# Performance work log

Hardware: AMD Instinct MI355X
Metric: run time of the kernel (lower is better)

## Reference

```python
import jax, jax.numpy as jnp
import numpy as np

B, S, D, H, DFF = 8, 1024, 1024, 16, 4096
DK = D // H
EPS = 1e-6
NEG = -1e9


def setup_inputs() -> dict:
    key = jax.random.key(0)
    ks = jax.random.split(key, 8)
    x = jax.random.normal(ks[0], (B, S, D), dtype=jnp.float32)
    mask = jnp.ones((B, 1, 1, S), dtype=jnp.int32)
    s = 0.02
    wq = jax.random.normal(ks[1], (D, D), jnp.float32) * s
    wk = jax.random.normal(ks[2], (D, D), jnp.float32) * s
    wv = jax.random.normal(ks[3], (D, D), jnp.float32) * s
    wo = jax.random.normal(ks[4], (D, D), jnp.float32) * s
    bq = jnp.zeros((D,), jnp.float32); bk = jnp.zeros((D,), jnp.float32)
    bv = jnp.zeros((D,), jnp.float32); bo = jnp.zeros((D,), jnp.float32)
    w1 = jax.random.normal(ks[5], (D, DFF), jnp.float32) * s
    b1 = jnp.zeros((DFF,), jnp.float32)
    w2 = jax.random.normal(ks[6], (DFF, D), jnp.float32) * s
    b2 = jnp.zeros((D,), jnp.float32)
    g1 = jnp.array(1.0, jnp.float32); be1 = jnp.array(0.0, jnp.float32)
    g2 = jnp.array(1.0, jnp.float32); be2 = jnp.array(0.0, jnp.float32)
    return dict(x=x, mask=mask, wq=wq, bq=bq, wk=wk, bk=bk, wv=wv, bv=bv,
                wo=wo, bo=bo, w1=w1, b1=b1, w2=w2, b2=b2,
                g1=g1, be1=be1, g2=g2, be2=be2)


def layer_norm(x, gamma, beta):
    # repo quirk: unbiased std (ddof=1), scalar gamma/beta, divide by (std+eps)
    mean = jnp.mean(x, axis=-1, keepdims=True)
    std = jnp.std(x, axis=-1, keepdims=True, ddof=1)
    return gamma * (x - mean) / (std + EPS) + beta


def mha(x, mask, wq, bq, wk, bk, wv, bv, wo, bo):
    q = (x @ wq + bq).reshape(B, S, H, DK).transpose(0, 2, 1, 3)  # bhsd
    k = (x @ wk + bk).reshape(B, S, H, DK).transpose(0, 2, 1, 3)
    v = (x @ wv + bv).reshape(B, S, H, DK).transpose(0, 2, 1, 3)
    scores = jnp.einsum('bhqd,bhkd->bhqk', q, k) / jnp.sqrt(jnp.float32(DK))
    scores = jnp.where(mask == 0, NEG, scores)
    attn = jax.nn.softmax(scores, axis=-1)
    out = jnp.einsum('bhqk,bhkd->bhqd', attn, v)
    out = out.transpose(0, 2, 1, 3).reshape(B, S, D)
    return out @ wo + bo


def reference(x, mask, wq, bq, wk, bk, wv, bv, wo, bo, w1, b1, w2, b2, g1, be1, g2, be2):
    # pre-LN residual: x + sublayer(norm(x)); dropout inert at eval
    x = x + mha(layer_norm(x, g1, be1), mask, wq, bq, wk, bk, wv, bv, wo, bo)
    h = layer_norm(x, g2, be2)
    x = x + (jax.nn.relu(h @ w1 + b1) @ w2 + b2)
    return x
```

## Files before the change

### kernel.cpp

```cpp
#include <hip/hip_runtime.h>
#include <math.h>

typedef __bf16 bf16;
typedef float f32x4 __attribute__((ext_vector_type(4)));
typedef float f32x16 __attribute__((ext_vector_type(16)));
typedef bf16 bf16x8 __attribute__((ext_vector_type(8)));
typedef bf16 bf16x4 __attribute__((ext_vector_type(4)));
typedef unsigned int u32;
typedef unsigned int u32x2 __attribute__((ext_vector_type(2)));

#define DEV __device__ __forceinline__

constexpr int Ss = 1024, Dd = 1024;
constexpr float EPSf = 1e-6f;
constexpr float SM_SCALE = 0.125f * 1.4426950408889634f;

DEV void gl_lds16(const void* g, void* l) {
  __builtin_amdgcn_global_load_lds(
      (const __attribute__((address_space(1))) void*)g,
      (__attribute__((address_space(3))) void*)l, 16, 0, 0);
}

DEV u32 cvtpk(float lo, float hi) {
  u32 r;
  asm("v_cvt_pk_bf16_f32 %0, %1, %2" : "=v"(r) : "v"(lo), "v"(hi));
  return r;
}

__global__ __launch_bounds__(256) void transpose6_k(
    const float* __restrict__ i0, const float* __restrict__ i1,
    const float* __restrict__ i2, const float* __restrict__ i3,
    const float* __restrict__ i4, const float* __restrict__ i5,
    bf16* __restrict__ o0, bf16* __restrict__ o1, bf16* __restrict__ o2,
    bf16* __restrict__ o3, bf16* __restrict__ o4, bf16* __restrict__ o5) {
  __shared__ float t[64 * 65];
  const int bi = blockIdx.x;
  const float* in;
  bf16* out;
  int R, C, local, sh;
  if (bi < 1024) {
    const int j = bi >> 8;
    local = bi & 255; R = 1024; C = 1024; sh = 4;
    in = (j == 0) ? i0 : (j == 1) ? i1 : (j == 2) ? i2 : i3;
    out = (j == 0) ? o0 : (j == 1) ? o1 : (j == 2) ? o2 : o3;
  } else if (bi < 2048) {
    local = bi - 1024; R = 1024; C = 4096; sh = 6; in = i4; out = o4;
  } else {
    local = bi - 2048; R = 4096; C = 1024; sh = 4; in = i5; out = o5;
  }
  const int nx = 1 << sh;
  const int bx = local & (nx - 1), by = local >> sh;
  const int tid = threadIdx.x;
  const int tx = tid & 63, ty = tid >> 6;
  const int r0 = by * 64, c0 = bx * 64;
#pragma unroll
  for (int i = 0; i < 16; i++) {
    int r = ty + i * 4;
    t[r * 65 + tx] = in[(size_t)(r0 + r) * C + c0 + tx];
  }
  __syncthreads();
#pragma unroll
  for (int i = 0; i < 16; i++) {
    int r = ty + i * 4;
    out[(size_t)(c0 + r) * R + r0 + tx] = (bf16)t[tx * 65 + r];
  }
}

__global__ __launch_bounds__(256) void ln_kernel(
    const float* __restrict__ in, bf16* __restrict__ out,
    const float* __restrict__ gp, const float* __restrict__ bp) {
  const int row = blockIdx.x;
  const int tid = threadIdx.x;
  float v[4];
  const float* p = in + (size_t)row * Dd + tid * 4;
#pragma unroll
  for (int i = 0; i < 4; i++) v[i] = p[i];
  float s = v[0] + v[1] + v[2] + v[3];
  float s2 = v[0] * v[0] + v[1] * v[1] + v[2] * v[2] + v[3] * v[3];
#pragma unroll
  for (int m = 1; m < 64; m <<= 1) {
    s += __shfl_xor(s, m, 64);
    s2 += __shfl_xor(s2, m, 64);
  }
  __shared__ float ls[4], ls2[4];
  if ((tid & 63) == 0) {
    ls[tid >> 6] = s;
    ls2[tid >> 6] = s2;
  }
  __syncthreads();
  s = ls[0] + ls[1] + ls[2] + ls[3];
  s2 = ls2[0] + ls2[1] + ls2[2] + ls2[3];
  float mean = s * (1.0f / Dd);
  float var = (s2 - (float)Dd * mean * mean) * (1.0f / (Dd - 1));
  var = fmaxf(var, 0.0f);
  float g = gp[0], be = bp[0];
  float rs = g / (sqrtf(var) + EPSf);
  bf16* q = out + (size_t)row * Dd + tid * 4;
#pragma unroll
  for (int i = 0; i < 4; i++) q[i] = (bf16)((v[i] - mean) * rs + be);
}

template <int EPI, int BK>
__global__ __launch_bounds__(256) void gemm_bt(
    const bf16* __restrict__ A, const bf16* __restrict__ Bt,
    const float* __restrict__ bias, const float* __restrict__ bias2,
    const float* __restrict__ bias3, const float* __restrict__ resid,
    bf16* __restrict__ vtb, void* __restrict__ Cout, int M, int N, int K,
    int sa, int sb) {
  __shared__ __attribute__((aligned(16))) char smem[2 * 128 * BK * 2];
  bf16* As = (bf16*)smem;
  bf16* Bs = (bf16*)(smem + 128 * BK * 2);
  constexpr int CPR = BK / 8;
  constexpr int RPJ = 256 / CPR;
  constexpr int NJ = BK / 16;
  const int tid = threadIdx.x;
  const int ln = tid & 63;
  const int wv = tid >> 6;
  const int wm = wv >> 1, wn = wv & 1;
  const int quad = ln >> 4, l16 = ln & 15;
  const int l7 = l16 & 7;
  const int nxg = gridDim.x;
  const int d = blockIdx.y * nxg + blockIdx.x;
  const int sseq = d >> 3;
  const int bxr = sseq % nxg;
  const int byr = (d & 7) + 8 * (sseq / nxg);
  const int m0 = byr * 128, n0 = bxr * 128;

  f32x4 acc[4][4];
#pragma unroll
  for (int i = 0; i < 4; i++)
#pragma unroll
    for (int j = 0; j < 4; j++) acc[i][j] = {0.f, 0.f, 0.f, 0.f};

  const int sr = tid / CPR;
  const int sc = (tid & (CPR - 1)) ^ (sr & 7);
  const size_t abase = (size_t)(m0 + sr) * sa + sc * 8;
  const size_t bbase = (size_t)(n0 + sr) * sb + sc * 8;

  for (int k0 = 0; k0 < K; k0 += BK) {
#pragma unroll
    for (int j = 0; j < NJ; j++) {
      gl_lds16(A + abase + (size_t)(j * RPJ) * sa + k0,
               (char*)As + j * 4096 + wv * 1024);
      gl_lds16(Bt + bbase + (size_t)(j * RPJ) * sb + k0,
               (char*)Bs + j * 4096 + wv * 1024);
    }
    __syncthreads();
#pragma unroll
    for (int kh = 0; kh < BK / 32; kh++) {
      bf16x8 af[4], bfr[4];
#pragma unroll
      for (int mi = 0; mi < 4; mi++)
        af[mi] = *(const bf16x8*)&As[(wm * 64 + mi * 16 + l16) * BK +
                                     ((kh * 4 + quad) ^ l7) * 8];
#pragma unroll
      for (int ni = 0; ni < 4; ni++)
        bfr[ni] = *(const bf16x8*)&Bs[(wn * 64 + ni * 16 + l16) * BK +
                                      ((kh * 4 + quad) ^ l7) * 8];
#pragma unroll
      for (int mi = 0; mi < 4; mi++)
#pragma unroll
        for (int ni = 0; ni < 4; ni++)
          acc[mi][ni] = __builtin_amdgcn_mfma_f32_16x16x32_bf16(
              af[mi], bfr[ni], acc[mi][ni], 0, 0, 0);
    }
    __syncthreads();
  }

  if constexpr (EPI == 4) {
    if (n0 < 2048) {
#pragma unroll
      for (int mi = 0; mi < 4; mi++) {
        const int m = m0 + wm * 64 + mi * 16 + quad * 4;
#pragma unroll
        for (int ni = 0; ni < 4; ni++) {
          const int n = n0 + wn * 64 + ni * 16 + l16;
          const float bvl = (n < 1024) ? bias[n] : bias2[n - 1024];
#pragma unroll
          for (int r = 0; r < 4; r++)
            ((bf16*)Cout)[(size_t)(m + r) * N + n] =
                (bf16)(acc[mi][ni][r] + bvl);
        }
      }
    } else {
      bf16* T = (bf16*)smem;
#pragma unroll
      for (int mi = 0; mi < 4; mi++) {
        const int ml = wm * 64 + mi * 16 + quad * 4;
        const int c = ml >> 3, hf = (ml >> 2) & 1;
#pragma unroll
        for (int ni = 0; ni < 4; ni++) {
          const int nl = wn * 64 + ni * 16 + l16;
          const float bvl = bias3[(n0 - 2048) + nl];
          bf16x4 tv;
#pragma unroll
          for (int r = 0; r < 4; r++) tv[r] = (bf16)(acc[mi][ni][r] + bvl);
          *(bf16x4*)&T[nl * 128 + ((c ^ (nl & 15)) << 3) + (hf << 2)] = tv;
        }
      }
      __syncthreads();
      const size_t vbase =
          ((size_t)(m0 >> 10) * 1024 + (n0 - 2048)) * Ss + (m0 & 1023);
#pragma unroll
      for (int p = 0; p < 8; p++) {
        const int row = p * 16 + (tid >> 4);
        const int k = tid & 15;
        bf16x8 vv = *(const bf16x8*)&T[row * 128 + ((k ^ (row & 15)) << 3)];
        *(bf16x8*)&vtb[vbase + (size_t)row * Ss + k * 8] = vv;
      }
    }
  } else {
#pragma unroll
    for (int mi = 0; mi < 4; mi++) {
      const int m = m0 + wm * 64 + mi * 16 + quad * 4;
#pragma unroll
      for (int ni = 0; ni < 4; ni++) {
        const int n = n0 + wn * 64 + ni * 16 + l16;
        float bvl = 0.0f;
        if constexpr (EPI != 3) bvl = bias[n];
#pragma unroll
        for (int r = 0; r < 4; r++) {
          float val = acc[mi][ni][r] + bvl;
          const size_t idx = (size_t)(m + r) * N + n;
          if constexpr (EPI == 1) {
            ((float*)Cout)[idx] = val + resid[idx];
          } else if constexpr (EPI == 2) {
            ((bf16*)Cout)[idx] = (bf16)fmaxf(val, 0.0f);
          } else {
            ((float*)Cout)[idx] = val + resid[idx];
          }
        }
      }
    }
  }
}

__global__ __launch_bounds__(512) void gemm256_relu(
    const bf16* __restrict__ A, const bf16* __restrict__ Bt,
    const float* __restrict__ bias, bf16* __restrict__ Cout, int M, int N,
    int K, int sa, int sb) {
  __shared__ __attribute__((aligned(16))) char smem[131072];
  const int tid = threadIdx.x;
  const int ln = tid & 63;
  const int wv = tid >> 6;
  const int wm = wv >> 2, wn = wv & 3;
  const int quad = ln >> 4, l16 = ln & 15;
  const int l7 = l16 & 7;
  const int nxg = gridDim.x;
  const int d = blockIdx.y * nxg + blockIdx.x;
  const int sseq = d >> 3;
  const int bxr = sseq % nxg;
  const int byr = (d & 7) + 8 * (sseq / nxg);
  const int m0 = byr * 256, n0 = bxr * 256;

  f32x4 acc[8][4];
#pragma unroll
  for (int i = 0; i < 8; i++)
#pragma unroll
    for (int j = 0; j < 4; j++) acc[i][j] = {0.f, 0.f, 0.f, 0.f};

  const int sr = tid >> 3;
  const int sc = (tid & 7) ^ (sr & 7);
  const size_t abase = (size_t)(m0 + sr) * sa + sc * 8;
  const size_t bbase = (size_t)(n0 + sr) * sb + sc * 8;
  const int w8 = tid >> 6;

  const int nt = K >> 6;
  int cur = 0;

  {
#pragma unroll
    for (int j = 0; j < 4; j++) {
      gl_lds16(A + abase + (size_t)(j * 64) * sa,
               smem + j * 8192 + w8 * 1024);
      gl_lds16(Bt + bbase + (size_t)(j * 64) * sb,
               smem + 32768 + j * 8192 + w8 * 1024);
    }
  }

  for (int t = 0; t < nt; ++t) {
    if (t + 1 < nt) {
      char* ldst = smem + (cur ^ 1) * 65536;
      const int koff = (t + 1) * 64;
#pragma unroll
      for (int j = 0; j < 4; j++) {
        gl_lds16(A + abase + (size_t)(j * 64) * sa + koff,
                 ldst + j * 8192 + w8 * 1024);
        gl_lds16(Bt + bbase + (size_t)(j * 64) * sb + koff,
                 ldst + 32768 + j * 8192 + w8 * 1024);
      }
      asm volatile("s_waitcnt vmcnt(8)" ::: "memory");
    } else {
      asm volatile("s_waitcnt vmcnt(0)" ::: "memory");
    }
    __builtin_amdgcn_s_barrier();

    const bf16* As = (const bf16*)(smem + cur * 65536);
    const bf16* Bs = (const bf16*)(smem + cur * 65536 + 32768);
    bf16x8 bfr[4][2];
#pragma unroll
    for (int ni = 0; ni < 4; ni++)
#pragma unroll
      for (int kh = 0; kh < 2; kh++)
        bfr[ni][kh] = *(const bf16x8*)&Bs[(wn * 64 + ni * 16 + l16) * 64 +
                                          (((kh * 4 + quad) ^ l7) * 8)];
#pragma unroll
    for (int p = 0; p < 4; p++) {
      bf16x8 af[2][2];
#pragma unroll
      for (int m2 = 0; m2 < 2; m2++)
#pragma unroll
        for (int kh = 0; kh < 2; kh++)
          af[m2][kh] =
              *(const bf16x8*)&As[(wm * 128 + (p * 2 + m2) * 16 + l16) * 64 +
                                  (((kh * 4 + quad) ^ l7) * 8)];
      __builtin_amdgcn_s_setprio(1);
#pragma unroll
      for (int m2 = 0; m2 < 2; m2++)
#pragma unroll
        for (int ni = 0; ni < 4; ni++)
#pragma unroll
          for (int kh = 0; kh < 2; kh++)
            acc[p * 2 + m2][ni] = __builtin_amdgcn_mfma_f32_16x16x32_bf16(
                af[m2][kh], bfr[ni][kh], acc[p * 2 + m2][ni], 0, 0, 0);
      __builtin_amdgcn_s_setprio(0);
    }
    __builtin_amdgcn_s_barrier();
    cur ^= 1;
  }

#pragma unroll
  for (int mi = 0; mi < 8; mi++) {
    const int m = m0 + wm * 128 + mi * 16 + quad * 4;
#pragma unroll
    for (int ni = 0; ni < 4; ni++) {
      const int n = n0 + wn * 64 + ni * 16 + l16;
      const float bvl = bias[n];
#pragma unroll
      for (int r = 0; r < 4; r++)
        Cout[(size_t)(m + r) * N + n] =
            (bf16)fmaxf(acc[mi][ni][r] + bvl, 0.0f);
    }
  }
}

__global__ __launch_bounds__(256) void attn_k(
    const bf16* __restrict__ qkv, const bf16* __restrict__ vt,
    const int* __restrict__ mask, bf16* __restrict__ ctx) {
  __shared__ __attribute__((aligned(16))) char smem[36864];
  __shared__ int Ft[16];
  bf16* Qs = (bf16*)smem;
  bf16* Ks = (bf16*)(smem + 16384);
  bf16* Vs = (bf16*)(smem + 24576);
  float* Fm = (float*)(smem + 32768);
  const int tid = threadIdx.x;
  const int l = tid & 63, w = tid >> 6;
  const int lq = l & 31, lh = l >> 5;
  const int lq7 = lq & 7;
  const int bh = blockIdx.x;
  const int b = bh >> 4, h = bh & 15;
  const int q0 = blockIdx.y * 128;
  const int sr = tid >> 3;
  const int sc = (tid & 7) ^ (sr & 7);

  if (tid < 16) Ft[tid] = 0;
  {
#pragma unroll
    for (int j = 0; j < 4; j++) {
      const size_t ga =
          (size_t)(b * Ss + q0 + j * 32 + sr) * 3072 + h * 64 + sc * 8;
      gl_lds16(qkv + ga, (char*)Qs + j * 4096 + w * 1024);
    }
  }
  __syncthreads();

  bf16x8 qf[4];
#pragma unroll
  for (int s = 0; s < 4; s++)
    qf[s] =
        *(const bf16x8*)&Qs[(w * 32 + lq) * 64 + (((s * 2 + lh) ^ lq7) * 8)];

  {
    const int4 mv = *(const int4*)&mask[b * Ss + tid * 4];
    const float ninf = -__builtin_inff();
    Fm[tid * 4 + 0] = mv.x ? 0.0f : ninf;
    Fm[tid * 4 + 1] = mv.y ? 0.0f : ninf;
    Fm[tid * 4 + 2] = mv.z ? 0.0f : ninf;
    Fm[tid * 4 + 3] = mv.w ? 0.0f : ninf;
    if (!(mv.x && mv.y && mv.z && mv.w)) atomicOr(&Ft[tid >> 4], 1);
  }

  f32x16 oacc[2];
#pragma unroll
  for (int d = 0; d < 2; d++)
#pragma unroll
    for (int r = 0; r < 16; r++) oacc[d][r] = 0.0f;
  float rsum = 0.0f;

  for (int kk0 = 0; kk0 < Ss; kk0 += 64) {
    {
#pragma unroll
      for (int j = 0; j < 2; j++) {
        const size_t ga = (size_t)(b * Ss + kk0 + j * 32 + sr) * 3072 + 1024 +
                          h * 64 + sc * 8;
        gl_lds16(qkv + ga, (char*)Ks + j * 4096 + w * 1024);
        const size_t gv = (size_t)(bh * 64 + j * 32 + sr) * Ss + kk0 + sc * 8;
        gl_lds16(vt + gv, (char*)Vs + j * 4096 + w * 1024);
      }
    }
    __syncthreads();

    f32x16 sacc[2];
#pragma unroll
    for (int kb = 0; kb < 2; kb++)
#pragma unroll
      for (int r = 0; r < 16; r++) sacc[kb][r] = 0.0f;

    __builtin_amdgcn_s_setprio(1);
#pragma unroll
    for (int kb = 0; kb < 2; kb++)
#pragma unroll
      for (int s = 0; s < 4; s++) {
        const bf16x8 kf = *(const bf16x8*)&Ks[(kb * 32 + lq) * 64 +
                                              (((s * 2 + lh) ^ lq7) * 8)];
        sacc[kb] = __builtin_amdgcn_mfma_f32_32x32x16_bf16(kf, qf[s],
                                                           sacc[kb], 0, 0, 0);
      }
    __builtin_amdgcn_s_setprio(0);

    if (__builtin_amdgcn_readfirstlane(Ft[kk0 >> 6])) {
#pragma unroll
      for (int kb = 0; kb < 2; kb++)
#pragma unroll
        for (int g = 0; g < 4; g++) {
          const f32x4 mv = *(const f32x4*)&Fm[kk0 + kb * 32 + 4 * lh + 8 * g];
#pragma unroll
          for (int j = 0; j < 4; j++)
            sacc[kb][g * 4 + j] = __builtin_amdgcn_exp2f(
                fmaf(sacc[kb][g * 4 + j], SM_SCALE, mv[j]));
        }
    } else {
#pragma unroll
      for (int kb = 0; kb < 2; kb++)
#pragma unroll
        for (int r = 0; r < 16; r++)
          sacc[kb][r] = __builtin_amdgcn_exp2f(sacc[kb][r] * SM_SCALE);
    }
#pragma unroll
    for (int kb = 0; kb < 2; kb++) {
      const float t0 = (sacc[kb][0] + sacc[kb][1]) + (sacc[kb][2] + sacc[kb][3]);
      const float t1 = (sacc[kb][4] + sacc[kb][5]) + (sacc[kb][6] + sacc[kb][7]);
      const float t2 =
          (sacc[kb][8] + sacc[kb][9]) + (sacc[kb][10] + sacc[kb][11]);
      const float t3 =
          (sacc[kb][12] + sacc[kb][13]) + (sacc[kb][14] + sacc[kb][15]);
      rsum += ((t0 + t1) + (t2 + t3));
    }

    __builtin_amdgcn_s_setprio(1);
#pragma unroll
    for (int t = 0; t < 4; t++) {
      const int kb = t >> 1, rb = (t & 1) * 8;
      u32 pa = cvtpk(sacc[kb][rb + 0], sacc[kb][rb + 1]);
      u32 pbv = cvtpk(sacc[kb][rb + 2], sacc[kb][rb + 3]);
      u32 pc = cvtpk(sacc[kb][rb + 4], sacc[kb][rb + 5]);
      u32 pd = cvtpk(sacc[kb][rb + 6], sacc[kb][rb + 7]);
      asm("v_permlane32_swap_b32 %0, %1" : "+v"(pa), "+v"(pc));
      asm("v_permlane32_swap_b32 %0, %1" : "+v"(pbv), "+v"(pd));
      union {
        u32 u[4];
        bf16x8 v;
      } pk;
      pk.u[0] = pa;
      pk.u[1] = pbv;
      pk.u[2] = pc;
      pk.u[3] = pd;
      const int vsw = ((t * 2 + lh) ^ lq7) * 8;
      const bf16x8 vf0 = *(const bf16x8*)&Vs[lq * 64 + vsw];
      const bf16x8 vf1 = *(const bf16x8*)&Vs[(32 + lq) * 64 + vsw];
      oacc[0] =
          __builtin_amdgcn_mfma_f32_32x32x16_bf16(vf0, pk.v, oacc[0], 0, 0, 0);
      oacc[1] =
          __builtin_amdgcn_mfma_f32_32x32x16_bf16(vf1, pk.v, oacc[1], 0, 0, 0);
    }
    __builtin_amdgcn_s_setprio(0);
    __syncthreads();
  }

  float xs = rsum, ys = rsum;
  asm("v_permlane32_swap_b32 %0, %1" : "+v"(xs), "+v"(ys));
  const float inv = 1.0f / (xs + ys);

  bf16* Tb = (bf16*)(smem + w * 4608);
#pragma unroll
  for (int dblk = 0; dblk < 2; dblk++)
#pragma unroll
    for (int g = 0; g < 4; g++) {
      const u32 lo =
          cvtpk(oacc[dblk][g * 4 + 0] * inv, oacc[dblk][g * 4 + 1] * inv);
      const u32 hi =
          cvtpk(oacc[dblk][g * 4 + 2] * inv, oacc[dblk][g * 4 + 3] * inv);
      u32x2 pr2;
      pr2[0] = lo;
      pr2[1] = hi;
      const int dbase = dblk * 32 + 8 * g + 4 * lh;
      *(u32x2*)&Tb[lq * 72 + dbase] = pr2;
    }
  __syncthreads();
#pragma unroll
  for (int p = 0; p < 4; p++) {
    const int row = p * 8 + (l >> 3);
    const int ch = l & 7;
    const bf16x8 vv = *(const bf16x8*)&Tb[row * 72 + ch * 8];
    *(bf16x8*)&ctx[(size_t)(b * Ss + q0 + w * 32 + row) * Dd + h * 64 +
                   ch * 8] = vv;
  }
}

extern "C" void kernel_launch(void* const* d_in, const int* in_sizes, int n_in,
                              void* d_out, int out_size, void* d_ws,
                              size_t ws_size, hipStream_t stream) {
  (void)in_sizes; (void)n_in; (void)out_size;
  const float* x = (const float*)d_in[0];
  const int* mask = (const int*)d_in[1];
  const float* wq = (const float*)d_in[2];
  const float* bq = (const float*)d_in[3];
  const float* wk = (const float*)d_in[4];
  const float* bk = (const float*)d_in[5];
  const float* wvw = (const float*)d_in[6];
  const float* bv = (const float*)d_in[7];
  const float* wo = (const float*)d_in[8];
  const float* bo = (const float*)d_in[9];
  const float* w1 = (const float*)d_in[10];
  const float* b1 = (const float*)d_in[11];
  const float* w2 = (const float*)d_in[12];
  const float* b2 = (const float*)d_in[13];
  const float* g1 = (const float*)d_in[14];
  const float* be1 = (const float*)d_in[15];
  const float* g2 = (const float*)d_in[16];
  const float* be2 = (const float*)d_in[17];
  float* out = (float*)d_out;

  char* ws = (char*)d_ws;
  const size_t MB = 1024 * 1024;
  bf16* w1T = (bf16*)(ws + 0 * MB);
  bf16* w2T = (bf16*)(ws + 8 * MB);
  bf16* wqkvT = (bf16*)(ws + 16 * MB);
  bf16* woT = (bf16*)(ws + 22 * MB);
  bf16* lnb = (bf16*)(ws + 24 * MB);
  bf16* qkv = (bf16*)(ws + 40 * MB);
  bf16* vtb = (bf16*)(ws + 88 * MB);
  float* x1 = (float*)(ws + 40 * MB);
  bf16* ctx = lnb;

  dim3 blk(256);
  transpose6_k<<<3072, blk, 0, stream>>>(
      wq, wk, wvw, wo, w1, w2, wqkvT, wqkvT + (size_t)1024 * 1024,
      wqkvT + (size_t)2048 * 1024, woT, w1T, w2T);
  ln_kernel<<<8192, blk, 0, stream>>>(x, lnb, g1, be1);
  gemm_bt<4, 64><<<dim3(24, 64), blk, 0, stream>>>(
      lnb, wqkvT, bq, bk, bv, nullptr, vtb, qkv, 8192, 3072, 1024, 1024, 1024);
  attn_k<<<dim3(128, 8), blk, 0, stream>>>(qkv, vtb, mask, ctx);
  gemm_bt<1, 128><<<dim3(8, 64), blk, 0, stream>>>(
      ctx, woT, bo, nullptr, nullptr, x, nullptr, x1, 8192, 1024, 1024, 1024,
      1024);
  ln_kernel<<<8192, blk, 0, stream>>>(x1, lnb, g2, be2);

  if (ws_size >= 136 * MB) {
    bf16* mid = (bf16*)(ws + 72 * MB);
    gemm256_relu<<<dim3(16, 32), dim3(512), 0, stream>>>(
        lnb, w1T, b1, mid, 8192, 4096, 1024, 1024, 1024);
    gemm_bt<1, 128><<<dim3(8, 64), blk, 0, stream>>>(
        mid, w2T, b2, nullptr, nullptr, x1, nullptr, out, 8192, 1024, 4096,
        4096, 4096);
  } else {
    bf16* mid = (bf16*)(ws + 72 * MB);
    gemm256_relu<<<dim3(8, 32), dim3(512), 0, stream>>>(
        lnb, w1T, b1, mid, 8192, 2048, 1024, 1024, 1024);
    gemm_bt<1, 128><<<dim3(8, 64), blk, 0, stream>>>(
        mid, w2T, b2, nullptr, nullptr, x1, nullptr, out, 8192, 1024, 2048,
        2048, 4096);
    gemm256_relu<<<dim3(8, 32), dim3(512), 0, stream>>>(
        lnb, w1T + (size_t)2048 * 1024, b1 + 2048, mid, 8192, 2048, 1024,
        1024, 1024);
    gemm_bt<3, 128><<<dim3(8, 64), blk, 0, stream>>>(
        mid, w2T + 2048, nullptr, nullptr, nullptr, out, nullptr, out, 8192,
        1024, 2048, 2048, 4096);
  }
}
```

Baseline: 442.9 us.

## Interleave global prefetch with MFMA in four quadrant phases of the FFN GEMM

Restructures the K-loop of the bias+ReLU GEMM into four quadrant phases, each loading a subset of A/B fragments from LDS, issuing a slice of the next tile's global-to-LDS loads, and running an MFMA block. This replaces issuing all prefetch loads up front and then computing. The goal is to spread memory traffic across the compute phases and hide load latency. It adds barriers per phase, and the vmcnt accounting now depends on exact load ordering.

```diff
diff --git a/kernel.cpp b/kernel.cpp
--- a/kernel.cpp
+++ b/kernel.cpp
@@ -277,53 +277,130 @@
                smem + 32768 + j * 8192 + w8 * 1024);
     }
   }
+  asm volatile("s_waitcnt vmcnt(0)" ::: "memory");
+  __builtin_amdgcn_s_barrier();
 
   for (int t = 0; t < nt; ++t) {
-    if (t + 1 < nt) {
-      char* ldst = smem + (cur ^ 1) * 65536;
-      const int koff = (t + 1) * 64;
-#pragma unroll
-      for (int j = 0; j < 4; j++) {
-        gl_lds16(A + abase + (size_t)(j * 64) * sa + koff,
-                 ldst + j * 8192 + w8 * 1024);
-        gl_lds16(Bt + bbase + (size_t)(j * 64) * sb + koff,
-                 ldst + 32768 + j * 8192 + w8 * 1024);
-      }
-      asm volatile("s_waitcnt vmcnt(8)" ::: "memory");
+    const bf16* As = (const bf16*)(smem + cur * 65536);
+    const bf16* Bs = (const bf16*)(smem + cur * 65536 + 32768);
+    char* ldst = smem + (cur ^ 1) * 65536;
+    const bool pf = (t + 1 < nt);
+    const int koff = (t + 1) * 64;
+
+    bf16x8 af[4][2], bfr[2][2];
+
+#pragma unroll
+    for (int mf = 0; mf < 4; mf++)
+#pragma unroll
+      for (int kh = 0; kh < 2; kh++)
+        af[mf][kh] = *(const bf16x8*)&As[(wm * 128 + mf * 16 + l16) * 64 +
+                                         (((kh * 4 + quad) ^ l7) * 8)];
+#pragma unroll
+    for (int nf = 0; nf < 2; nf++)
+#pragma unroll
+      for (int kh = 0; kh < 2; kh++)
+        bfr[nf][kh] = *(const bf16x8*)&Bs[(wn * 64 + nf * 16 + l16) * 64 +
+                                          (((kh * 4 + quad) ^ l7) * 8)];
+    if (pf) {
+      gl_lds16(Bt + bbase + koff, ldst + 32768 + w8 * 1024);
+      gl_lds16(Bt + bbase + (size_t)64 * sb + koff,
+               ldst + 32768 + 8192 + w8 * 1024);
+    }
+    __builtin_amdgcn_s_barrier();
+    __builtin_amdgcn_s_setprio(1);
+#pragma unroll
+    for (int mf = 0; mf < 4; mf++)
+#pragma unroll
+      for (int nf = 0; nf < 2; nf++)
+#pragma unroll
+        for (int kh = 0; kh < 2; kh++)
+          acc[mf][nf] = __builtin_amdgcn_mfma_f32_16x16x32_bf16(
+              af[mf][kh], bfr[nf][kh], acc[mf][nf], 0, 0, 0);
+    __builtin_amdgcn_s_setprio(0);
+    if (pf) {
+      asm volatile("s_waitcnt vmcnt(2)" ::: "memory");
     } else {
       asm volatile("s_waitcnt vmcnt(0)" ::: "memory");
     }
     __builtin_amdgcn_s_barrier();
 
-    const bf16* As = (const bf16*)(smem + cur * 65536);
-    const bf16* Bs = (const bf16*)(smem + cur * 65536 + 32768);
-    bf16x8 bfr[4][2];
-#pragma unroll
-    for (int ni = 0; ni < 4; ni++)
+#pragma unroll
+    for (int mf = 0; mf < 4; mf++)
 #pragma unroll
       for (int kh = 0; kh < 2; kh++)
-        bfr[ni][kh] = *(const bf16x8*)&Bs[(wn * 64 + ni * 16 + l16) * 64 +
-                                          (((kh * 4 + quad) ^ l7) * 8)];
-#pragma unroll
-    for (int p = 0; p < 4; p++) {
-      bf16x8 af[2][2];
-#pragma unroll
-      for (int m2 = 0; m2 < 2; m2++)
+        af[mf][kh] =
+            *(const bf16x8*)&As[(wm * 128 + 64 + mf * 16 + l16) * 64 +
+                                (((kh * 4 + quad) ^ l7) * 8)];
+    if (pf) {
+      gl_lds16(Bt + bbase + (size_t)128 * sb + koff,
+               ldst + 32768 + 16384 + w8 * 1024);
+      gl_lds16(Bt + bbase + (size_t)192 * sb + koff,
+               ldst + 32768 + 24576 + w8 * 1024);
+    }
+    __builtin_amdgcn_s_barrier();
+    __builtin_amdgcn_s_setprio(1);
+#pragma unroll
+    for (int mf = 0; mf < 4; mf++)
+#pragma unroll
+      for (int nf = 0; nf < 2; nf++)
 #pragma unroll
         for (int kh = 0; kh < 2; kh++)
-          af[m2][kh] =
-              *(const bf16x8*)&As[(wm * 128 + (p * 2 + m2) * 16 + l16) * 64 +
-                                  (((kh * 4 + quad) ^ l7) * 8)];
-      __builtin_amdgcn_s_setprio(1);
-#pragma unroll
-      for (int m2 = 0; m2 < 2; m2++)
-#pragma unroll
-        for (int ni = 0; ni < 4; ni++)
-#pragma unroll
-          for (int kh = 0; kh < 2; kh++)
-            acc[p * 2 + m2][ni] = __builtin_amdgcn_mfma_f32_16x16x32_bf16(
-                af[m2][kh], bfr[ni][kh], acc[p * 2 + m2][ni], 0, 0, 0);
-      __builtin_amdgcn_s_setprio(0);
+          acc[4 + mf][nf] = __builtin_amdgcn_mfma_f32_16x16x32_bf16(
+              af[mf][kh], bfr[nf][kh], acc[4 + mf][nf], 0, 0, 0);
+    __builtin_amdgcn_s_setprio(0);
+    __builtin_amdgcn_s_barrier();
+
+#pragma unroll
+    for (int nf = 0; nf < 2; nf++)
+#pragma unroll
+      for (int kh = 0; kh < 2; kh++)
+        bfr[nf][kh] =
+            *(const bf16x8*)&Bs[(wn * 64 + 32 + nf * 16 + l16) * 64 +
+                                (((kh * 4 + quad) ^ l7) * 8)];
+    if (pf) {
+      gl_lds16(A + abase + koff, ldst + w8 * 1024);
+      gl_lds16(A + abase + (size_t)128 * sa + koff,
+               ldst + 16384 + w8 * 1024);
+    }
+    __builtin_amdgcn_s_barrier();
+    __builtin_amdgcn_s_setprio(1);
+#pragma unroll
+    for (int mf = 0; mf < 4; mf++)
+#pragma unroll
+      for (int nf = 0; nf < 2; nf++)
+#pragma unroll
+        for (int kh = 0; kh < 2; kh++)
+          acc[4 + mf][2 + nf] = __builtin_amdgcn_mfma_f32_16x16x32_bf16(
+              af[mf][kh], bfr[nf][kh], acc[4 + mf][2 + nf], 0, 0, 0);
+    __builtin_amdgcn_s_setprio(0);
+    __builtin_amdgcn_s_barrier();
+
+#pragma unroll
+    for (int mf = 0; mf < 4; mf++)
+#pragma unroll
+      for (int kh = 0; kh < 2; kh++)
+        af[mf][kh] = *(const bf16x8*)&As[(wm * 128 + mf * 16 + l16) * 64 +
+                                         (((kh * 4 + quad) ^ l7) * 8)];
+    if (pf) {
+      gl_lds16(A + abase + (size_t)64 * sa + koff, ldst + 8192 + w8 * 1024);
+      gl_lds16(A + abase + (size_t)192 * sa + koff,
+               ldst + 24576 + w8 * 1024);
+    }
+    __builtin_amdgcn_s_barrier();
+    __builtin_amdgcn_s_setprio(1);
+#pragma unroll
+    for (int mf = 0; mf < 4; mf++)
+#pragma unroll
+      for (int nf = 0; nf < 2; nf++)
+#pragma unroll
+        for (int kh = 0; kh < 2; kh++)
+          acc[mf][2 + nf] = __builtin_amdgcn_mfma_f32_16x16x32_bf16(
+              af[mf][kh], bfr[nf][kh], acc[mf][2 + nf], 0, 0, 0);
+    __builtin_amdgcn_s_setprio(0);
+    if (pf) {
+      asm volatile("s_waitcnt vmcnt(2)" ::: "memory");
+    } else {
+      asm volatile("s_waitcnt vmcnt(0)" ::: "memory");
     }
     __builtin_amdgcn_s_barrier();
     cur ^= 1;
```

Result: slower. 454.2 us (+2.5%).
